# Performance work log

Hardware: AMD Instinct MI355X
Metric: run time of the kernel (lower is better)

Reference implementation:

```python
import jax, jax.numpy as jnp
import numpy as np

B, S, D = 2, 2048, 1024
H, KD, VD = 16, 64, 64

def setup_inputs() -> dict:
    key = jax.random.key(0)
    ks = jax.random.split(key, 6)
    sd = 1.0 / np.sqrt(D)
    x = jax.random.normal(ks[0], (B, S, D), dtype=jnp.float32)
    Wq = jax.random.uniform(ks[1], (D, KD * H), jnp.float32, -sd, sd)
    Wk = jax.random.uniform(ks[2], (D, KD * H), jnp.float32, -sd, sd)
    Wv = jax.random.uniform(ks[3], (D, VD * H), jnp.float32, -sd, sd)
    so = 1.0 / np.sqrt(VD * H)
    Wo = jax.random.uniform(ks[4], (VD * H, D), jnp.float32, -so, so)
    bo = jax.random.uniform(ks[5], (D,), jnp.float32, -so, so)
    return {"x": x, "Wq": Wq, "Wk": Wk, "Wv": Wv, "Wo": Wo, "bo": bo}

def reference(x, Wq, Wk, Wv, Wo, bo):
    b, s, _ = x.shape
    q = (x @ Wq).reshape(b, s, H, KD).transpose(0, 2, 1, 3)  # bhsd
    k = (x @ Wk).reshape(b, s, H, KD).transpose(0, 2, 1, 3)
    v = (x @ Wv).reshape(b, s, H, VD).transpose(0, 2, 1, 3)
    attn = jnp.einsum('bhqd,bhkd->bhqk', q, k) / np.sqrt(KD).astype(np.float32)
    attn = jax.nn.softmax(attn, axis=-1)
    out = jnp.einsum('bhqk,bhkd->bhqd', attn, v)
    out = out.transpose(0, 2, 1, 3).reshape(b, s, H * VD)
    return out @ Wo + bo
```

## Files before the change

### kernel.cpp

```cpp
#include <hip/hip_runtime.h>
#include <cstdint>
#include <cstddef>

typedef unsigned short u16;
typedef unsigned int u32;
typedef __attribute__((ext_vector_type(4))) float f32x4;
typedef __attribute__((ext_vector_type(4))) short s16x4;
typedef __attribute__((ext_vector_type(8))) short s16x8;
typedef __attribute__((ext_vector_type(8))) __bf16 bf16x8;

#define DEV __device__ __forceinline__
#define GLOAD_LDS(src, dst)                                        \
  __builtin_amdgcn_global_load_lds(                                \
      (const __attribute__((address_space(1))) void*)(src),        \
      (__attribute__((address_space(3))) void*)(dst), 16, 0, 0)

constexpr int BATCH = 2;
constexpr int SEQ   = 2048;
constexpr int DM    = 1024;
constexpr int NH    = 16;
constexpr int HD    = 64;
constexpr int NTOK  = BATCH * SEQ;


DEV u16 f2b(float x) {
  unsigned u = __builtin_bit_cast(unsigned, x);
  u = u + 0x7FFFu + ((u >> 16) & 1u);
  return (u16)(u >> 16);
}

DEV u32 pkbf(float lo, float hi) {
  u32 a = __builtin_bit_cast(u32, lo) + 0x8000u;
  u32 b = __builtin_bit_cast(u32, hi) + 0x8000u;
  return __builtin_amdgcn_perm(b, a, 0x07060302u);
}

DEV float fexp2(float x) {
#if __has_builtin(__builtin_amdgcn_exp2f)
  return __builtin_amdgcn_exp2f(x);
#else
  float r;
  asm volatile("v_exp_f32 %0, %1" : "=v"(r) : "v"(x));
  return r;
#endif
}

DEV bf16x8 ld128(const u16* p) { return __builtin_bit_cast(bf16x8, *(const s16x8*)p); }

__global__ void k_cvt(const float* __restrict__ x, u16* __restrict__ y) {
  const int G = blockIdx.x * 256 + threadIdx.x;
  const int row = G >> 7, g = G & 127;
  const float* xp = x + (size_t)row * DM + (g >> 2) * 32 + (g & 3) * 4;
  float4 a = *(const float4*)xp;
  float4 b = *(const float4*)(xp + 16);
  union { u16 h[8]; s16x8 v; } o;
  o.h[0] = f2b(a.x); o.h[1] = f2b(a.y); o.h[2] = f2b(a.z); o.h[3] = f2b(a.w);
  o.h[4] = f2b(b.x); o.h[5] = f2b(b.y); o.h[6] = f2b(b.z); o.h[7] = f2b(b.w);
  *(s16x8*)(y + (size_t)row * DM + g * 8) = o.v;
}

__global__ void k_wtrans(const float* __restrict__ w0, const float* __restrict__ w1,
                         const float* __restrict__ w2, const float* __restrict__ w3,
                         u16* __restrict__ t0, u16* __restrict__ t1,
                         u16* __restrict__ t2, u16* __restrict__ t3) {
  const float* w; u16* t;
  switch (blockIdx.z) {
    case 0: w = w0; t = t0; break;
    case 1: w = w1; t = t1; break;
    case 2: w = w2; t = t2; break;
    default: w = w3; t = t3; break;
  }
  __shared__ float tile[32][33];
  int tx = threadIdx.x & 31, ty = threadIdx.x >> 5;
  int r0 = blockIdx.y * 32, c0 = blockIdx.x * 32;
#pragma unroll
  for (int i = 0; i < 4; i++)
    tile[ty + 8 * i][tx] = w[(size_t)(r0 + ty + 8 * i) * DM + c0 + tx];
  __syncthreads();
  const int dtx = (((tx >> 2) & 1) << 4) | (((tx >> 3) & 3) << 2) | (tx & 3);
#pragma unroll
  for (int i = 0; i < 4; i++)
    t[(size_t)(c0 + ty + 8 * i) * DM + r0 + tx] = f2b(tile[dtx][ty + 8 * i]);
}

template <int MODE, int BM>
__global__ __launch_bounds__(256) void k_gemm(
    const u16* __restrict__ A,
    const u16* __restrict__ B0, const u16* __restrict__ B1, const u16* __restrict__ B2,
    u16* __restrict__ C0, u16* __restrict__ C1, u16* __restrict__ C2,
    float* __restrict__ Cf, const float* __restrict__ bias) {
  constexpr int N = 1024, K = 1024, BN = 128, BK = 64;
  constexpr int AM = BM / 32;
  const u16* Bt = B0;
  u16* Cb = C0;
  int z = 0;
  if (MODE == 0) {
    z = blockIdx.z;
    Bt = (z == 0) ? B0 : (z == 1) ? B1 : B2;
    Cb = (z == 0) ? C0 : (z == 1) ? C1 : C2;
  }
  const int m0 = blockIdx.y * BM, n0 = blockIdx.x * BN;
  __shared__ u16 As[BM][BK];
  __shared__ u16 Bs[BN][BK];
  const int t = threadIdx.x;
  const int wid = t >> 6, lane = t & 63, lr = lane & 15, lg = lane >> 4;
  const int wm = wid >> 1, wn = wid & 1;
  const int l8 = lane >> 3;
  const int scol = (((lane & 7) ^ l8) << 3);
  const int g0 = (lg ^ (lr & 7)) << 3;
  const int g1 = ((4 + lg) ^ (lr & 7)) << 3;

  const f32x4 z4 = {0.f, 0.f, 0.f, 0.f};
  f32x4 acc[AM][4];
#pragma unroll
  for (int a = 0; a < AM; a++)
#pragma unroll
    for (int fb = 0; fb < 4; fb++) acc[a][fb] = z4;

  const u16* Ap = A + (size_t)m0 * K;
  const u16* Bp = Bt + (size_t)n0 * K;

  for (int kt = 0; kt < K; kt += BK) {
#pragma unroll
    for (int s2 = 0; s2 < AM; s2++) {
      const int seg = wid * AM + s2;
      GLOAD_LDS(Ap + (size_t)(seg * 8 + l8) * K + kt + scol, &As[seg * 8][0]);
    }
#pragma unroll
    for (int s2 = 0; s2 < 4; s2++) {
      const int seg = wid * 4 + s2;
      GLOAD_LDS(Bp + (size_t)(seg * 8 + l8) * K + kt + scol, &Bs[seg * 8][0]);
    }
    __syncthreads();
#pragma unroll
    for (int kk = 0; kk < 2; kk++) {
      const int gk = kk ? g1 : g0;
      bf16x8 af[AM], bfr[4];
#pragma unroll
      for (int a = 0; a < AM; a++)
        af[a] = ld128(&As[wm * (AM * 16) + a * 16 + lr][0] + gk);
#pragma unroll
      for (int fb = 0; fb < 4; fb++)
        bfr[fb] = ld128(&Bs[wn * 64 + fb * 16 + lr][0] + gk);
#pragma unroll
      for (int a = 0; a < AM; a++)
#pragma unroll
        for (int fb = 0; fb < 4; fb++)
          acc[a][fb] = __builtin_amdgcn_mfma_f32_16x16x32_bf16(af[a], bfr[fb], acc[a][fb], 0, 0, 0);
    }
    __syncthreads();
  }
#pragma unroll
  for (int a = 0; a < AM; a++) {
#pragma unroll
    for (int fb = 0; fb < 4; fb++) {
      const int c = n0 + wn * 64 + fb * 16 + lr;
      const int cst = (MODE == 0 && z < 2)
                          ? ((c & ~31) | ((lr >> 2) << 3) | ((fb & 1) << 2) | (lr & 3))
                          : c;
      float bb = (MODE == 1) ? bias[c] : 0.f;
#pragma unroll
      for (int j = 0; j < 4; j++) {
        const int r = m0 + wm * (AM * 16) + a * 16 + lg * 4 + j;
        if (MODE == 0)
          Cb[(size_t)r * N + cst] = f2b(acc[a][fb][j]);
        else
          Cf[(size_t)r * N + c] = acc[a][fb][j] + bb;
      }
    }
  }
}

__global__ void k_vtrans(const u16* __restrict__ V, u16* __restrict__ Vt) {
  const int bh = blockIdx.y, b = bh >> 4, h = bh & 15;
  const int t0 = blockIdx.x * 64;
  __shared__ u16 tile[64][72];
  const int t = threadIdx.x;
#pragma unroll
  for (int p = 0; p < 2; p++) {
    int c = p * 256 + t;
    int row = c >> 3, off = (c & 7) * 8;
    *(s16x8*)&tile[row][off] =
        *(const s16x8*)&V[(size_t)(b * SEQ + t0 + row) * DM + h * HD + off];
  }
  __syncthreads();
#pragma unroll
  for (int p = 0; p < 2; p++) {
    int c = p * 256 + t;
    int vd = c >> 3, off = (c & 7) * 8;
    union { u16 a[8]; s16x8 v; } u;
    const int base = (off & ~31) + ((off >> 3) & 3) * 4;
#pragma unroll
    for (int j = 0; j < 8; j++) {
      const int key_local = base + (j >> 2) * 16 + (j & 3);
      u.a[j] = tile[key_local][vd];
    }
    *(s16x8*)&Vt[(size_t)(bh * HD + vd) * SEQ + t0 + off] = u.v;
  }
}

__global__ __launch_bounds__(256) void k_attn(const u16* __restrict__ Q, const u16* __restrict__ K,
                                              const u16* __restrict__ Vt, u16* __restrict__ O) {
  __shared__ u16 KS[2][64][64];
  __shared__ u16 VS[2][64][64];
  const int flat = blockIdx.x;
  const int swz = (flat & 7) * 64 + (flat >> 3);
  const int bh = swz >> 4, b = bh >> 4, h = bh & 15;
  const int q0 = (swz & 15) * 128;
  const int t = threadIdx.x, w = t >> 6, lane = t & 63, lr = lane & 15, lg = lane >> 4;
  const int l8 = lane >> 3;
  const int scol = (((lane & 7) ^ l8) << 3);
  const int g0 = (lg ^ (lr & 7)) << 3;
  const int g1 = ((4 + lg) ^ (lr & 7)) << 3;
  const float SCL = 0.18033688f;
  const float MS  = 12.0f * SCL;

  bf16x8 qf[2][2];
#pragma unroll
  for (int qb = 0; qb < 2; qb++) {
    const u16* qp = Q + (size_t)(b * SEQ + q0 + w * 32 + qb * 16 + lr) * DM + h * HD;
    qf[qb][0] = ld128(qp + lg * 8);
    qf[qb][1] = ld128(qp + 32 + lg * 8);
  }

  float l[2] = {0.f, 0.f};
  const f32x4 z4 = {0.f, 0.f, 0.f, 0.f};
  f32x4 o[2][4];
#pragma unroll
  for (int qb = 0; qb < 2; qb++)
#pragma unroll
    for (int v = 0; v < 4; v++) o[qb][v] = z4;

#define STAGE(buf, kv)                                                                  \
  {                                                                                     \
    _Pragma("unroll") for (int s2 = 0; s2 < 2; s2++) {                                  \
      const int seg = w * 2 + s2;                                                       \
      const int row = seg * 8 + l8;                                                     \
      GLOAD_LDS(K + (size_t)(b * SEQ + (kv) + row) * DM + h * HD + scol,                \
                &KS[buf][seg * 8][0]);                                                  \
      GLOAD_LDS(Vt + (size_t)(bh * HD + row) * SEQ + (kv) + scol, &VS[buf][seg * 8][0]);\
    }                                                                                   \
  }

  STAGE(0, 0);
  __syncthreads();

  for (int it = 0; it < SEQ / 64; it++) {
    const int cur = it & 1;
    if (it < SEQ / 64 - 1) STAGE(cur ^ 1, (it + 1) * 64);

    f32x4 s[2][4];
#pragma unroll
    for (int qb = 0; qb < 2; qb++)
#pragma unroll
      for (int n = 0; n < 4; n++) s[qb][n] = z4;
    __builtin_amdgcn_s_setprio(1);
#pragma unroll
    for (int kk = 0; kk < 2; kk++) {
      const int gk = kk ? g1 : g0;
      bf16x8 kf[4];
#pragma unroll
      for (int n = 0; n < 4; n++) kf[n] = ld128(&KS[cur][16 * n + lr][0] + gk);
#pragma unroll
      for (int qb = 0; qb < 2; qb++)
#pragma unroll
        for (int n = 0; n < 4; n++)
          s[qb][n] = __builtin_amdgcn_mfma_f32_16x16x32_bf16(kf[n], qf[qb][kk], s[qb][n], 0, 0, 0);
    }
    __builtin_amdgcn_s_setprio(0);

    bf16x8 pf[2][2];
#pragma unroll
    for (int qb = 0; qb < 2; qb++) {
      union { u32 u[8]; bf16x8 v[2]; } pk;
      float r = 0.f;
#pragma unroll
      for (int n = 0; n < 4; n++) {
        float p0 = fexp2(fmaf(s[qb][n][0], SCL, -MS));
        float p1 = fexp2(fmaf(s[qb][n][1], SCL, -MS));
        float p2 = fexp2(fmaf(s[qb][n][2], SCL, -MS));
        float p3 = fexp2(fmaf(s[qb][n][3], SCL, -MS));
        r += (p0 + p1) + (p2 + p3);
        pk.u[n * 2 + 0] = pkbf(p0, p1);
        pk.u[n * 2 + 1] = pkbf(p2, p3);
      }
      l[qb] += r;
      pf[qb][0] = pk.v[0];
      pf[qb][1] = pk.v[1];
    }

    __builtin_amdgcn_s_setprio(1);
#pragma unroll
    for (int kc = 0; kc < 2; kc++) {
      const int gk = kc ? g1 : g0;
      bf16x8 vf[4];
#pragma unroll
      for (int v = 0; v < 4; v++) vf[v] = ld128(&VS[cur][16 * v + lr][0] + gk);
#pragma unroll
      for (int qb = 0; qb < 2; qb++)
#pragma unroll
        for (int v = 0; v < 4; v++)
          o[qb][v] = __builtin_amdgcn_mfma_f32_16x16x32_bf16(pf[qb][kc], vf[v], o[qb][v], 0, 0, 0);
    }
    __builtin_amdgcn_s_setprio(0);
    __syncthreads();
  }

#pragma unroll
  for (int qb = 0; qb < 2; qb++) {
    l[qb] += __shfl_xor(l[qb], 16);
    l[qb] += __shfl_xor(l[qb], 32);
    float linv[4];
#pragma unroll
    for (int j = 0; j < 4; j++) linv[j] = 1.0f / __shfl(l[qb], 4 * lg + j);
#pragma unroll
    for (int v = 0; v < 4; v++) {
      const int cst = h * HD + (v >> 1) * 32 + ((lr >> 2) << 3) + ((v & 1) << 2) + (lr & 3);
#pragma unroll
      for (int j = 0; j < 4; j++)
        O[(size_t)(b * SEQ + q0 + w * 32 + qb * 16 + 4 * lg + j) * DM + cst] =
            f2b(o[qb][v][j] * linv[j]);
    }
  }
#undef STAGE
}

extern "C" void kernel_launch(void* const* d_in, const int* in_sizes, int n_in,
                              void* d_out, int out_size, void* d_ws, size_t ws_size,
                              hipStream_t stream) {
  const float* x  = (const float*)d_in[0];
  const float* Wq = (const float*)d_in[1];
  const float* Wk = (const float*)d_in[2];
  const float* Wv = (const float*)d_in[3];
  const float* Wo = (const float*)d_in[4];
  const float* bo = (const float*)d_in[5];
  float* out = (float*)d_out;

  char* ws = (char*)d_ws;
  const size_t MB = 1 << 20;
  u16* xb  = (u16*)(ws + 0 * MB);
  u16* WqT = (u16*)(ws + 8 * MB);
  u16* WkT = (u16*)(ws + 10 * MB);
  u16* WvT = (u16*)(ws + 12 * MB);
  u16* WoT = (u16*)(ws + 14 * MB);
  u16* Qb  = (u16*)(ws + 16 * MB);
  u16* Kb  = (u16*)(ws + 24 * MB);
  u16* Vb  = (u16*)(ws + 32 * MB);
  u16* Vtb = (u16*)(ws + 40 * MB);
  u16* Ob  = (u16*)(ws + 48 * MB);

  k_cvt<<<dim3(NTOK * DM / (256 * 8)), 256, 0, stream>>>(x, xb);
  k_wtrans<<<dim3(32, 32, 4), 256, 0, stream>>>(Wq, Wk, Wv, Wo, WqT, WkT, WvT, WoT);
  k_gemm<0, 128><<<dim3(8, 32, 3), 256, 0, stream>>>(xb, WqT, WkT, WvT, Qb, Kb, Vb, nullptr,
                                                     nullptr);
  k_vtrans<<<dim3(32, 32), 256, 0, stream>>>(Vb, Vtb);
  k_attn<<<dim3(512), 256, 0, stream>>>(Qb, Kb, Vtb, Ob);
  k_gemm<1, 64><<<dim3(8, 64, 1), 256, 0, stream>>>(Ob, WoT, nullptr, nullptr, nullptr, nullptr,
                                                    nullptr, out, bo);
}
```

Before: 194.1 us.

## Split attention KV range across two wave groups, MFMA row sums, hardware bf16 pack

The attention block doubles to 512 threads. Two halves of 4 waves each process disjoint halves of the key sequence for the same 128 queries, then merge partial outputs and row sums through LDS before normalising. The softmax denominator is now accumulated with an extra MFMA against a ones vector, replacing the scalar adds and cross-lane shuffles. The bf16 packing uses the v_cvt_pk_bf16_f32 instruction. This aims to raise occupancy and shorten the serial KV loop, at the cost of doubled LDS, an extra merge barrier, and a fixed max-shift softmax that is unchanged.

Result: faster. 173.7 us (-10.5%).

```diff
diff --git a/kernel.cpp b/kernel.cpp
--- a/kernel.cpp
+++ b/kernel.cpp
@@ -29,10 +29,10 @@
   return (u16)(u >> 16);
 }
 
-DEV u32 pkbf(float lo, float hi) {
-  u32 a = __builtin_bit_cast(u32, lo) + 0x8000u;
-  u32 b = __builtin_bit_cast(u32, hi) + 0x8000u;
-  return __builtin_amdgcn_perm(b, a, 0x07060302u);
+DEV u32 cvtpk(float lo, float hi) {
+  u32 r;
+  asm("v_cvt_pk_bf16_f32 %0, %1, %2" : "=v"(r) : "v"(lo), "v"(hi));
+  return r;
 }
 
 DEV float fexp2(float x) {
@@ -199,15 +199,16 @@
   }
 }
 
-__global__ __launch_bounds__(256) void k_attn(const u16* __restrict__ Q, const u16* __restrict__ K,
+__global__ __launch_bounds__(512) void k_attn(const u16* __restrict__ Q, const u16* __restrict__ K,
                                               const u16* __restrict__ Vt, u16* __restrict__ O) {
-  __shared__ u16 KS[2][64][64];
-  __shared__ u16 VS[2][64][64];
+  __shared__ u16 KS[2][2][64][64];
+  __shared__ u16 VS[2][2][64][64];
   const int flat = blockIdx.x;
   const int swz = (flat & 7) * 64 + (flat >> 3);
   const int bh = swz >> 4, b = bh >> 4, h = bh & 15;
   const int q0 = (swz & 15) * 128;
   const int t = threadIdx.x, w = t >> 6, lane = t & 63, lr = lane & 15, lg = lane >> 4;
+  const int half = w >> 2, wsub = w & 3;
   const int l8 = lane >> 3;
   const int scol = (((lane & 7) ^ l8) << 3);
   const int g0 = (lg ^ (lr & 7)) << 3;
@@ -215,39 +216,45 @@
   const float SCL = 0.18033688f;
   const float MS  = 12.0f * SCL;
 
+  union { u32 u[4]; bf16x8 v; } ones_;
+#pragma unroll
+  for (int i = 0; i < 4; i++) ones_.u[i] = 0x3F803F80u;
+  const bf16x8 ones = ones_.v;
+
   bf16x8 qf[2][2];
 #pragma unroll
   for (int qb = 0; qb < 2; qb++) {
-    const u16* qp = Q + (size_t)(b * SEQ + q0 + w * 32 + qb * 16 + lr) * DM + h * HD;
+    const u16* qp = Q + (size_t)(b * SEQ + q0 + wsub * 32 + qb * 16 + lr) * DM + h * HD;
     qf[qb][0] = ld128(qp + lg * 8);
     qf[qb][1] = ld128(qp + 32 + lg * 8);
   }
 
-  float l[2] = {0.f, 0.f};
   const f32x4 z4 = {0.f, 0.f, 0.f, 0.f};
-  f32x4 o[2][4];
+  f32x4 o[2][4], ls[2] = {z4, z4};
 #pragma unroll
   for (int qb = 0; qb < 2; qb++)
 #pragma unroll
     for (int v = 0; v < 4; v++) o[qb][v] = z4;
 
-#define STAGE(buf, kv)                                                                  \
-  {                                                                                     \
-    _Pragma("unroll") for (int s2 = 0; s2 < 2; s2++) {                                  \
-      const int seg = w * 2 + s2;                                                       \
-      const int row = seg * 8 + l8;                                                     \
-      GLOAD_LDS(K + (size_t)(b * SEQ + (kv) + row) * DM + h * HD + scol,                \
-                &KS[buf][seg * 8][0]);                                                  \
-      GLOAD_LDS(Vt + (size_t)(bh * HD + row) * SEQ + (kv) + scol, &VS[buf][seg * 8][0]);\
-    }                                                                                   \
+#define STAGE(buf, it_)                                                                  \
+  {                                                                                      \
+    const int kvb = half * 1024 + (it_) * 64;                                            \
+    _Pragma("unroll") for (int s2 = 0; s2 < 2; s2++) {                                   \
+      const int seg = wsub * 2 + s2;                                                     \
+      const int row = seg * 8 + l8;                                                      \
+      GLOAD_LDS(K + (size_t)(b * SEQ + kvb + row) * DM + h * HD + scol,                  \
+                &KS[buf][half][seg * 8][0]);                                             \
+      GLOAD_LDS(Vt + (size_t)(bh * HD + row) * SEQ + kvb + scol,                         \
+                &VS[buf][half][seg * 8][0]);                                             \
+    }                                                                                    \
   }
 
   STAGE(0, 0);
   __syncthreads();
 
-  for (int it = 0; it < SEQ / 64; it++) {
+  for (int it = 0; it < 16; it++) {
     const int cur = it & 1;
-    if (it < SEQ / 64 - 1) STAGE(cur ^ 1, (it + 1) * 64);
+    if (it < 15) STAGE(cur ^ 1, it + 1);
 
     f32x4 s[2][4];
 #pragma unroll
@@ -260,7 +267,7 @@
       const int gk = kk ? g1 : g0;
       bf16x8 kf[4];
 #pragma unroll
-      for (int n = 0; n < 4; n++) kf[n] = ld128(&KS[cur][16 * n + lr][0] + gk);
+      for (int n = 0; n < 4; n++) kf[n] = ld128(&KS[cur][half][16 * n + lr][0] + gk);
 #pragma unroll
       for (int qb = 0; qb < 2; qb++)
 #pragma unroll
@@ -273,18 +280,15 @@
 #pragma unroll
     for (int qb = 0; qb < 2; qb++) {
       union { u32 u[8]; bf16x8 v[2]; } pk;
-      float r = 0.f;
 #pragma unroll
       for (int n = 0; n < 4; n++) {
         float p0 = fexp2(fmaf(s[qb][n][0], SCL, -MS));
         float p1 = fexp2(fmaf(s[qb][n][1], SCL, -MS));
         float p2 = fexp2(fmaf(s[qb][n][2], SCL, -MS));
         float p3 = fexp2(fmaf(s[qb][n][3], SCL, -MS));
-        r += (p0 + p1) + (p2 + p3);
-        pk.u[n * 2 + 0] = pkbf(p0, p1);
-        pk.u[n * 2 + 1] = pkbf(p2, p3);
+        pk.u[n * 2 + 0] = cvtpk(p0, p1);
+        pk.u[n * 2 + 1] = cvtpk(p2, p3);
       }
-      l[qb] += r;
       pf[qb][0] = pk.v[0];
       pf[qb][1] = pk.v[1];
     }
@@ -295,31 +299,56 @@
       const int gk = kc ? g1 : g0;
       bf16x8 vf[4];
 #pragma unroll
-      for (int v = 0; v < 4; v++) vf[v] = ld128(&VS[cur][16 * v + lr][0] + gk);
-#pragma unroll
-      for (int qb = 0; qb < 2; qb++)
+      for (int v = 0; v < 4; v++) vf[v] = ld128(&VS[cur][half][16 * v + lr][0] + gk);
+#pragma unroll
+      for (int qb = 0; qb < 2; qb++) {
 #pragma unroll
         for (int v = 0; v < 4; v++)
           o[qb][v] = __builtin_amdgcn_mfma_f32_16x16x32_bf16(pf[qb][kc], vf[v], o[qb][v], 0, 0, 0);
+        ls[qb] = __builtin_amdgcn_mfma_f32_16x16x32_bf16(pf[qb][kc], ones, ls[qb], 0, 0, 0);
+      }
     }
     __builtin_amdgcn_s_setprio(0);
     __syncthreads();
   }
 
-#pragma unroll
-  for (int qb = 0; qb < 2; qb++) {
-    l[qb] += __shfl_xor(l[qb], 16);
-    l[qb] += __shfl_xor(l[qb], 32);
-    float linv[4];
-#pragma unroll
-    for (int j = 0; j < 4; j++) linv[j] = 1.0f / __shfl(l[qb], 4 * lg + j);
-#pragma unroll
-    for (int v = 0; v < 4; v++) {
-      const int cst = h * HD + (v >> 1) * 32 + ((lr >> 2) << 3) + ((v & 1) << 2) + (lr & 3);
-#pragma unroll
-      for (int j = 0; j < 4; j++)
-        O[(size_t)(b * SEQ + q0 + w * 32 + qb * 16 + 4 * lg + j) * DM + cst] =
-            f2b(o[qb][v][j] * linv[j]);
+  float* mb = ((w & 2) ? (float*)&VS[0][0][0][0] : (float*)&KS[0][0][0][0]) +
+              (((w & 1) << 6) + lane) * 40;
+  if (half) {
+#pragma unroll
+    for (int qb = 0; qb < 2; qb++) {
+#pragma unroll
+      for (int v = 0; v < 4; v++)
+#pragma unroll
+        for (int j = 0; j < 4; j++) mb[qb * 16 + v * 4 + j] = o[qb][v][j];
+#pragma unroll
+      for (int j = 0; j < 4; j++) mb[32 + qb * 4 + j] = ls[qb][j];
+    }
+  }
+  __syncthreads();
+  if (!half) {
+#pragma unroll
+    for (int qb = 0; qb < 2; qb++) {
+#pragma unroll
+      for (int v = 0; v < 4; v++)
+#pragma unroll
+        for (int j = 0; j < 4; j++) o[qb][v][j] += mb[qb * 16 + v * 4 + j];
+#pragma unroll
+      for (int j = 0; j < 4; j++) ls[qb][j] += mb[32 + qb * 4 + j];
+    }
+#pragma unroll
+    for (int qb = 0; qb < 2; qb++) {
+      float linv[4];
+#pragma unroll
+      for (int j = 0; j < 4; j++) linv[j] = 1.0f / ls[qb][j];
+#pragma unroll
+      for (int v = 0; v < 4; v++) {
+        const int cst = h * HD + (v >> 1) * 32 + ((lr >> 2) << 3) + ((v & 1) << 2) + (lr & 3);
+#pragma unroll
+        for (int j = 0; j < 4; j++)
+          O[(size_t)(b * SEQ + q0 + wsub * 32 + qb * 16 + 4 * lg + j) * DM + cst] =
+              f2b(o[qb][v][j] * linv[j]);
+      }
     }
   }
 #undef STAGE
@@ -354,7 +383,7 @@
   k_gemm<0, 128><<<dim3(8, 32, 3), 256, 0, stream>>>(xb, WqT, WkT, WvT, Qb, Kb, Vb, nullptr,
                                                      nullptr);
   k_vtrans<<<dim3(32, 32), 256, 0, stream>>>(Vb, Vtb);
-  k_attn<<<dim3(512), 256, 0, stream>>>(Qb, Kb, Vtb, Ob);
+  k_attn<<<dim3(512), 512, 0, stream>>>(Qb, Kb, Vtb, Ob);
   k_gemm<1, 64><<<dim3(8, 64, 1), 256, 0, stream>>>(Ob, WoT, nullptr, nullptr, nullptr, nullptr,
                                                     nullptr, out, bo);
 }
```
